# Performance work log

Measured on AMD Instinct MI355X. Metric: run time of the kernel, lower is better.

The kernel has to match this reference:

```python
import jax, jax.numpy as jnp
import numpy as np

N_NODES = 100_000
N_EDGES = 1_600_000
NUM_BASIS = 10
MAX_RADIUS = 5.0
NUM_NEIGHBORS = 10.0


def _sph_harm_lmax2(u):
    # u: [E,3] unit vectors. e3nn real spherical harmonics, lmax=2,
    # normalization='component' (each l-block has per-component unit variance).
    x, y, z = u[:, 0], u[:, 1], u[:, 2]
    s3 = jnp.sqrt(3.0)
    s5 = jnp.sqrt(5.0)
    s15 = jnp.sqrt(15.0)
    return jnp.stack([
        jnp.ones_like(x),                      # l=0
        s3 * x, s3 * y, s3 * z,                # l=1
        s15 * x * z,                           # l=2
        s15 * x * y,
        s5 * (y * y - 0.5 * (x * x + z * z)),
        s15 * y * z,
        0.5 * s15 * (z * z - x * x),
    ], axis=-1)                                # [E,9]


def _soft_one_hot_smooth_finite(r):
    # e3nn soft_one_hot_linspace(r, 0, max_radius, num_basis, 'smooth_finite', cutoff=True)
    vals = jnp.linspace(0.0, MAX_RADIUS, NUM_BASIS + 2)
    step = vals[1] - vals[0]
    vals = vals[1:-1]
    d = (r[:, None] - vals[None, :]) / step    # [E,num_basis]
    inside = jnp.abs(d) < 1.0
    d2 = jnp.where(inside, d * d, 0.0)
    y = 1.14136 * jnp.exp(2.0) * jnp.exp(-1.0 / (1.0 - d2))
    return jnp.where(inside, y, 0.0)


def setup_inputs() -> dict:
    key = jax.random.key(0)
    k1, k2, k3, k4, k5, k6 = jax.random.split(key, 6)
    return {
        "pos": jax.random.normal(k1, (N_NODES, 3), dtype=jnp.float32),
        "node_feats": jax.random.normal(k2, (N_NODES, 9), dtype=jnp.float32),
        "W1": jax.random.normal(k3, (NUM_BASIS, 16), dtype=jnp.float32),
        "W2": jax.random.normal(k4, (16, 3), dtype=jnp.float32),
        "edge_src": jax.random.randint(k5, (N_EDGES,), 0, N_NODES, dtype=jnp.int32),
        "edge_dst": jax.random.randint(k6, (N_EDGES,), 0, N_NODES, dtype=jnp.int32),
    }


def reference(pos, node_feats, W1, W2, edge_src, edge_dst):
    # gather: per-edge geometry
    edge_vec = pos[edge_dst] - pos[edge_src]          # [E,3]
    r = jnp.linalg.norm(edge_vec, axis=-1)            # [E]
    u = edge_vec / (r[:, None] + 1e-12)
    sh = _sph_harm_lmax2(u)                           # [E,9]

    # radial embedding -> small MLP -> per-edge tensor-product weights (weight_numel=3)
    emb = _soft_one_hot_smooth_finite(r) * jnp.sqrt(jnp.float32(NUM_BASIS))
    h = jax.nn.relu(emb @ W1 / jnp.sqrt(jnp.float32(NUM_BASIS))) * jnp.sqrt(2.0)
    w = h @ W2 / jnp.sqrt(16.0)                       # [E,3]

    # FullyConnectedTensorProduct('1x0e+1x1o+1x2e', sh, '1x0e'), shared_weights=False
    # paths: 0e*0e->0e, 1o*1o->0e, 2e*2e->0e ; w3j(l,l,0)=I/sqrt(2l+1); fan-in 3 paths.
    x1 = node_feats[edge_src]                         # [E,9]
    path_s = x1[:, 0] * sh[:, 0]
    path_p = jnp.sum(x1[:, 1:4] * sh[:, 1:4], axis=-1) / jnp.sqrt(3.0)
    path_d = jnp.sum(x1[:, 4:9] * sh[:, 4:9], axis=-1) / jnp.sqrt(5.0)
    msg = (w[:, 0] * path_s + w[:, 1] * path_p + w[:, 2] * path_d) / jnp.sqrt(3.0)

    # scatter-aggregate messages to destination nodes
    node_out = jax.ops.segment_sum(msg, edge_dst, num_segments=N_NODES)
    node_out = node_out / jnp.sqrt(jnp.float32(NUM_NEIGHBORS))
    return node_out[:, None]                          # [N,1] scalar ('1x0e') per node
```

## Files before the change

### kernel.cpp

```cpp
#include <hip/hip_runtime.h>
#include <math.h>

#define N_NODES 100000
#define N_EDGES 1600000

#define BUCKETS 8
#define SUBS 64
#define BUCKET_NODES (N_NODES / BUCKETS)
#define SLICE (N_EDGES / SUBS)

__global__ __launch_bounds__(256) void pack_kernel(
    const float* __restrict__ pos,
    const float* __restrict__ feats,
    float4* __restrict__ posw,
    float4* __restrict__ featsw)
{
    const int i = blockIdx.x * blockDim.x + threadIdx.x;
    if (i >= N_NODES) return;
    const float* p = pos + 3 * i;
    const float* f = feats + 9 * i;
    posw[i]           = make_float4(p[0], p[1], p[2], f[0]);
    featsw[2 * i + 0] = make_float4(f[1], f[2], f[3], f[4]);
    featsw[2 * i + 1] = make_float4(f[5], f[6], f[7], f[8]);
}

__device__ __forceinline__ float edge_msg(
    const float4 a, const float4 b, const float4 c, const float4 pd,
    const float* __restrict__ sW1, const float* __restrict__ sW2)
{
    const float vx = pd.x - a.x;
    const float vy = pd.y - a.y;
    const float vz = pd.z - a.z;

    const float r   = sqrtf(vx * vx + vy * vy + vz * vz);
    const float inv = 1.0f / (r + 1e-12f);
    const float x = vx * inv, y = vy * inv, z = vz * inv;

    const float s3  = 1.7320508075688772f;
    const float s5  = 2.23606797749979f;
    const float s15 = 3.872983346207417f;
    const float sh1 = s3 * x;
    const float sh2 = s3 * y;
    const float sh3 = s3 * z;
    const float sh4 = s15 * x * z;
    const float sh5 = s15 * x * y;
    const float sh6 = s5 * (y * y - 0.5f * (x * x + z * z));
    const float sh7 = s15 * y * z;
    const float sh8 = 0.5f * s15 * (z * z - x * x);

    const float q = r * 2.2f;
    const int   k = (int)floorf(q);
    int   b0 = k - 1, b1 = k;
    const float d0 = q - (float)k;
    const float d1 = d0 - 1.0f;
    const float A = 8.43357307f;
    float e0 = 0.0f, e1 = 0.0f;
    if (b0 >= 0 && b0 < 10) {
        const float dd = d0 * d0;
        if (dd < 1.0f) e0 = A * expf(-1.0f / (1.0f - dd));
    }
    if (b1 >= 0 && b1 < 10) {
        const float dd = d1 * d1;
        if (dd < 1.0f) e1 = A * expf(-1.0f / (1.0f - dd));
    }
    b0 = (b0 >= 0 && b0 < 10) ? b0 : 0;
    b1 = (b1 >= 0 && b1 < 10) ? b1 : 0;

    const float* w1r0 = sW1 + b0 * 17;
    const float* w1r1 = sW1 + b1 * 17;
    float acc0 = 0.0f, acc1 = 0.0f, acc2 = 0.0f;
#pragma unroll
    for (int j = 0; j < 16; ++j) {
        const float hj = fmaxf(e0 * w1r0[j] + e1 * w1r1[j], 0.0f);
        acc0 = fmaf(hj, sW2[j * 3 + 0], acc0);
        acc1 = fmaf(hj, sW2[j * 3 + 1], acc1);
        acc2 = fmaf(hj, sW2[j * 3 + 2], acc2);
    }

    const float path_s = a.w;
    const float path_p = (b.x * sh1 + b.y * sh2 + b.z * sh3) * 0.5773502691896258f;
    const float path_d = (b.w * sh4 + c.x * sh5 + c.y * sh6
                        + c.z * sh7 + c.w * sh8) * 0.4472135954999579f;

    const float FINAL = 0.06454972243679028f;
    return (acc0 * path_s + acc1 * path_p + acc2 * path_d) * FINAL;
}

__global__ __launch_bounds__(256) void msg_kernel(
    const float4* __restrict__ posw,
    const float4* __restrict__ featsw,
    const float* __restrict__ W1,
    const float* __restrict__ W2,
    const int* __restrict__ edge_src,
    const int* __restrict__ edge_dst,
    float* __restrict__ msg)
{
    __shared__ float sW1[10 * 17];
    __shared__ float sW2[16 * 3];
    const int t = threadIdx.x;
    if (t < 160) sW1[(t >> 4) * 17 + (t & 15)] = W1[t];
    if (t < 48)  sW2[t] = W2[t];
    __syncthreads();

    const int e = blockIdx.x * blockDim.x + t;
    if (e >= N_EDGES) return;

    const int s = edge_src[e];
    const int d = edge_dst[e];
    const float4 a = posw[s];
    const float4 b = featsw[2 * s + 0];
    const float4 c = featsw[2 * s + 1];
    const float4 p = posw[d];
    msg[e] = edge_msg(a, b, c, p, sW1, sW2);
}

__global__ __launch_bounds__(256) void scatter_kernel(
    const int* __restrict__ edge_dst,
    const float* __restrict__ msg,
    float* __restrict__ slabs)
{
    __shared__ float acc[BUCKET_NODES];
    const int b = blockIdx.x >> 6;
    const int s = blockIdx.x & (SUBS - 1);
    const int base = b * BUCKET_NODES;
    const int t = threadIdx.x;

    for (int i = t; i < BUCKET_NODES; i += 256) acc[i] = 0.0f;
    __syncthreads();

    const int e0 = s * SLICE;
    const int4*   d4 = (const int4*)(edge_dst + e0);
    const float4* m4 = (const float4*)(msg + e0);
    for (int i = t; i < SLICE / 4; i += 256) {
        const int4   d = d4[i];
        const float4 m = m4[i];
        if ((unsigned)(d.x - base) < (unsigned)BUCKET_NODES) atomicAdd(&acc[d.x - base], m.x);
        if ((unsigned)(d.y - base) < (unsigned)BUCKET_NODES) atomicAdd(&acc[d.y - base], m.y);
        if ((unsigned)(d.z - base) < (unsigned)BUCKET_NODES) atomicAdd(&acc[d.z - base], m.z);
        if ((unsigned)(d.w - base) < (unsigned)BUCKET_NODES) atomicAdd(&acc[d.w - base], m.w);
    }
    __syncthreads();

    float* slab = slabs + ((size_t)blockIdx.x) * BUCKET_NODES;
    for (int i = t; i < BUCKET_NODES; i += 256) slab[i] = acc[i];
}

__global__ __launch_bounds__(256) void reduce_kernel(
    const float* __restrict__ slabs, float* __restrict__ out)
{
    const int n = blockIdx.x * blockDim.x + threadIdx.x;
    if (n >= N_NODES) return;
    const int b = n / BUCKET_NODES;
    const int i = n - b * BUCKET_NODES;
    const float* sl = slabs + (size_t)b * SUBS * BUCKET_NODES + i;
    float sum = 0.0f;
#pragma unroll
    for (int k = 0; k < SUBS; ++k) sum += sl[(size_t)k * BUCKET_NODES];
    out[n] = sum;
}

__global__ __launch_bounds__(256) void edge_kernel_direct(
    const float* __restrict__ pos,
    const float* __restrict__ node_feats,
    const float* __restrict__ W1,
    const float* __restrict__ W2,
    const int*   __restrict__ edge_src,
    const int*   __restrict__ edge_dst,
    float* __restrict__ out)
{
    __shared__ float sW1[10 * 17];
    __shared__ float sW2[16 * 3];
    const int t = threadIdx.x;
    if (t < 160) sW1[(t >> 4) * 17 + (t & 15)] = W1[t];
    if (t < 48)  sW2[t] = W2[t];
    __syncthreads();

    const int e = blockIdx.x * blockDim.x + t;
    if (e >= N_EDGES) return;

    const int src = edge_src[e];
    const int dst = edge_dst[e];
    const float* ps = pos + 3 * src;
    const float* pd = pos + 3 * dst;
    const float* xf = node_feats + 9 * src;
    const float4 a = make_float4(ps[0], ps[1], ps[2], xf[0]);
    const float4 b = make_float4(xf[1], xf[2], xf[3], xf[4]);
    const float4 c = make_float4(xf[5], xf[6], xf[7], xf[8]);
    const float4 pdv = make_float4(pd[0], pd[1], pd[2], 0.0f);
    const float m = edge_msg(a, b, c, pdv, sW1, sW2);
    unsafeAtomicAdd(out + dst, m);
}

extern "C" void kernel_launch(void* const* d_in, const int* in_sizes, int n_in,
                              void* d_out, int out_size, void* d_ws, size_t ws_size,
                              hipStream_t stream) {
    const float* pos        = (const float*)d_in[0];
    const float* node_feats = (const float*)d_in[1];
    const float* W1         = (const float*)d_in[2];
    const float* W2         = (const float*)d_in[3];
    const int*   edge_src   = (const int*)d_in[4];
    const int*   edge_dst   = (const int*)d_in[5];
    float* out = (float*)d_out;

    const size_t posw_bytes   = (size_t)N_NODES * sizeof(float4);
    const size_t featsw_bytes = (size_t)N_NODES * 2 * sizeof(float4);
    const size_t msg_bytes    = (size_t)N_EDGES * sizeof(float);
    const size_t slab_bytes   = (size_t)BUCKETS * SUBS * BUCKET_NODES * sizeof(float);
    const size_t need = posw_bytes + featsw_bytes + msg_bytes + slab_bytes;

    if (ws_size >= need) {
        char* w = (char*)d_ws;
        float4* posw   = (float4*)w;                      w += posw_bytes;
        float4* featsw = (float4*)w;                      w += featsw_bytes;
        float*  msg    = (float*)w;                       w += msg_bytes;
        float*  slabs  = (float*)w;

        pack_kernel<<<(N_NODES + 255) / 256, 256, 0, stream>>>(pos, node_feats, posw, featsw);
        msg_kernel<<<(N_EDGES + 255) / 256, 256, 0, stream>>>(
            posw, featsw, W1, W2, edge_src, edge_dst, msg);
        scatter_kernel<<<BUCKETS * SUBS, 256, 0, stream>>>(edge_dst, msg, slabs);
        reduce_kernel<<<(N_NODES + 255) / 256, 256, 0, stream>>>(slabs, out);
    } else {
        hipMemsetAsync(out, 0, N_NODES * sizeof(float), stream);
        edge_kernel_direct<<<(N_EDGES + 255) / 256, 256, 0, stream>>>(
            pos, node_feats, W1, W2, edge_src, edge_dst, out);
    }
}
```

Measured before the change: 142.4 us.

## Bucket edge messages by destination during message compute to avoid repeated scatter scans

```diff
diff --git a/kernel.cpp b/kernel.cpp
--- a/kernel.cpp
+++ b/kernel.cpp
@@ -5,9 +5,10 @@
 #define N_EDGES 1600000
 
 #define BUCKETS 8
-#define SUBS 64
+#define GSPLIT 32
 #define BUCKET_NODES (N_NODES / BUCKETS)
-#define SLICE (N_EDGES / SUBS)
+#define NSEG (BUCKETS * GSPLIT)
+#define CAP 8192
 
 __global__ __launch_bounds__(256) void pack_kernel(
     const float* __restrict__ pos,
@@ -86,14 +87,15 @@
     return (acc0 * path_s + acc1 * path_p + acc2 * path_d) * FINAL;
 }
 
-__global__ __launch_bounds__(256) void msg_kernel(
+__global__ __launch_bounds__(256) void msg_part_kernel(
     const float4* __restrict__ posw,
     const float4* __restrict__ featsw,
     const float* __restrict__ W1,
     const float* __restrict__ W2,
     const int* __restrict__ edge_src,
     const int* __restrict__ edge_dst,
-    float* __restrict__ msg)
+    int*  __restrict__ counters,
+    int2* __restrict__ segs)
 {
     __shared__ float sW1[10 * 17];
     __shared__ float sW2[16 * 3];
@@ -102,46 +104,60 @@
     if (t < 48)  sW2[t] = W2[t];
     __syncthreads();
 
-    const int e = blockIdx.x * blockDim.x + t;
-    if (e >= N_EDGES) return;
-
+    const int e = blockIdx.x * 256 + t;
     const int s = edge_src[e];
     const int d = edge_dst[e];
-    const float4 a = posw[s];
-    const float4 b = featsw[2 * s + 0];
-    const float4 c = featsw[2 * s + 1];
-    const float4 p = posw[d];
-    msg[e] = edge_msg(a, b, c, p, sW1, sW2);
+    const float4 a  = posw[s];
+    const float4 bb = featsw[2 * s + 0];
+    const float4 cc = featsw[2 * s + 1];
+    const float4 p  = posw[d];
+    const float m = edge_msg(a, bb, cc, p, sW1, sW2);
+
+    const int g        = blockIdx.x & (GSPLIT - 1);
+    const int mybucket = d / BUCKET_NODES;
+    const int local    = d - mybucket * BUCKET_NODES;
+    const int lane     = t & 63;
+
+#pragma unroll
+    for (int b = 0; b < BUCKETS; ++b) {
+        const unsigned long long mask = __ballot(mybucket == b);
+        if (mask == 0ull) continue;
+        const int leader = __ffsll((unsigned long long)mask) - 1;
+        int base = 0;
+        if (lane == leader)
+            base = atomicAdd(&counters[b * GSPLIT + g], (int)__popcll(mask));
+        base = __shfl(base, leader);
+        if (mybucket == b) {
+            const int rank = (int)__popcll(mask & ((1ull << lane) - 1ull));
+            const int slot = base + rank;
+            if (slot < CAP)
+                segs[(size_t)(b * GSPLIT + g) * CAP + slot] =
+                    make_int2(local, __float_as_int(m));
+        }
+    }
 }
 
 __global__ __launch_bounds__(256) void scatter_kernel(
-    const int* __restrict__ edge_dst,
-    const float* __restrict__ msg,
+    const int* __restrict__ counters,
+    const int2* __restrict__ segs,
     float* __restrict__ slabs)
 {
     __shared__ float acc[BUCKET_NODES];
-    const int b = blockIdx.x >> 6;
-    const int s = blockIdx.x & (SUBS - 1);
-    const int base = b * BUCKET_NODES;
+    const int seg = blockIdx.x;
     const int t = threadIdx.x;
-
     for (int i = t; i < BUCKET_NODES; i += 256) acc[i] = 0.0f;
     __syncthreads();
 
-    const int e0 = s * SLICE;
-    const int4*   d4 = (const int4*)(edge_dst + e0);
-    const float4* m4 = (const float4*)(msg + e0);
-    for (int i = t; i < SLICE / 4; i += 256) {
-        const int4   d = d4[i];
-        const float4 m = m4[i];
-        if ((unsigned)(d.x - base) < (unsigned)BUCKET_NODES) atomicAdd(&acc[d.x - base], m.x);
-        if ((unsigned)(d.y - base) < (unsigned)BUCKET_NODES) atomicAdd(&acc[d.y - base], m.y);
-        if ((unsigned)(d.z - base) < (unsigned)BUCKET_NODES) atomicAdd(&acc[d.z - base], m.z);
-        if ((unsigned)(d.w - base) < (unsigned)BUCKET_NODES) atomicAdd(&acc[d.w - base], m.w);
-    }
-    __syncthreads();
-
-    float* slab = slabs + ((size_t)blockIdx.x) * BUCKET_NODES;
+    int count = counters[seg];
+    if (count > CAP) count = CAP;
+    const int2* sp = segs + (size_t)seg * CAP;
+    for (int i = t; i < count; i += 256) {
+        const int2 pr = sp[i];
+        atomicAdd(&acc[pr.x], __int_as_float(pr.y));
+    }
+    __syncthreads();
+
+    float* slab = slabs + (size_t)seg * BUCKET_NODES;
     for (int i = t; i < BUCKET_NODES; i += 256) slab[i] = acc[i];
 }
 
@@ -152,10 +168,10 @@
     if (n >= N_NODES) return;
     const int b = n / BUCKET_NODES;
     const int i = n - b * BUCKET_NODES;
-    const float* sl = slabs + (size_t)b * SUBS * BUCKET_NODES + i;
+    const float* sl = slabs + ((size_t)b * GSPLIT) * BUCKET_NODES + i;
     float sum = 0.0f;
 #pragma unroll
-    for (int k = 0; k < SUBS; ++k) sum += sl[(size_t)k * BUCKET_NODES];
+    for (int g = 0; g < GSPLIT; ++g) sum += sl[(size_t)g * BUCKET_NODES];
     out[n] = sum;
 }
 
@@ -204,21 +220,25 @@
 
     const size_t posw_bytes   = (size_t)N_NODES * sizeof(float4);
     const size_t featsw_bytes = (size_t)N_NODES * 2 * sizeof(float4);
-    const size_t msg_bytes    = (size_t)N_EDGES * sizeof(float);
-    const size_t slab_bytes   = (size_t)BUCKETS * SUBS * BUCKET_NODES * sizeof(float);
-    const size_t need = posw_bytes + featsw_bytes + msg_bytes + slab_bytes;
+    const size_t cnt_bytes    = (size_t)NSEG * sizeof(int);
+    const size_t cnt_pad      = 4096;
+    const size_t seg_bytes    = (size_t)NSEG * CAP * sizeof(int2);
+    const size_t slab_bytes   = (size_t)NSEG * BUCKET_NODES * sizeof(float);
+    const size_t need = posw_bytes + featsw_bytes + cnt_pad + seg_bytes + slab_bytes;
 
     if (ws_size >= need) {
         char* w = (char*)d_ws;
-        float4* posw   = (float4*)w;                      w += posw_bytes;
-        float4* featsw = (float4*)w;                      w += featsw_bytes;
-        float*  msg    = (float*)w;                       w += msg_bytes;
+        float4* posw   = (float4*)w;  w += posw_bytes;
+        float4* featsw = (float4*)w;  w += featsw_bytes;
+        int*    cnts   = (int*)w;     w += cnt_pad;
+        int2*   segs   = (int2*)w;    w += seg_bytes;
         float*  slabs  = (float*)w;
 
+        hipMemsetAsync(cnts, 0, cnt_bytes, stream);
         pack_kernel<<<(N_NODES + 255) / 256, 256, 0, stream>>>(pos, node_feats, posw, featsw);
-        msg_kernel<<<(N_EDGES + 255) / 256, 256, 0, stream>>>(
-            posw, featsw, W1, W2, edge_src, edge_dst, msg);
-        scatter_kernel<<<BUCKETS * SUBS, 256, 0, stream>>>(edge_dst, msg, slabs);
+        msg_part_kernel<<<N_EDGES / 256, 256, 0, stream>>>(
+            posw, featsw, W1, W2, edge_src, edge_dst, cnts, segs);
+        scatter_kernel<<<NSEG, 256, 0, stream>>>(cnts, segs, slabs);
         reduce_kernel<<<(N_NODES + 255) / 256, 256, 0, stream>>>(slabs, out);
     } else {
         hipMemsetAsync(out, 0, N_NODES * sizeof(float), stream);
```

New measurement: 396.4 us. 178% more time.
